# Kernel tuning notes

Measured on AMD Instinct MI355X. Metric: run time of the kernel, lower is better.

Reference implementation:

```python
import jax, jax.numpy as jnp
import numpy as np

K = 3
STRIDE = 1
PADDING = 1


def unfold(x, k, stride, padding):
    # torch.nn.functional.unfold: patches ordered (C, kh, kw), positions row-major
    N, C, H, W = x.shape
    xp = jnp.pad(x, ((0, 0), (0, 0), (padding, padding), (padding, padding)))
    H_out = (H - k + 2 * padding) // stride + 1
    W_out = (W - k + 2 * padding) // stride + 1
    patches = jnp.stack(
        [xp[:, :, i:i + stride * H_out:stride, j:j + stride * W_out:stride]
         for i in range(k) for j in range(k)],
        axis=2,
    )  # (N, C, k*k, H_out, W_out)
    return patches.reshape(N, C * k * k, H_out * W_out), H_out, W_out


def setup_inputs() -> dict:
    key = jax.random.key(0)
    k1, k2 = jax.random.split(key)
    x = jax.random.normal(k1, (16, 64, 14, 14), dtype=jnp.float32)
    W = jax.random.normal(k2, (64, 64, 3, 3), dtype=jnp.float32)
    return {"x": x, "W": W}


def reference(x, W):
    F_out = W.shape[0]
    X_col, H_out, W_out = unfold(x, K, STRIDE, PADDING)  # (N, D, P)
    W_col = W.reshape(F_out, -1)                          # (F, D)
    # AdderNet: out[n,f,p] = -sum_d |W[f,d] - X[n,d,p]|
    out = -jnp.sum(jnp.abs(W_col[None, :, :, None] - X_col[:, None, :, :]), axis=2)  # (N, F, P)
    return out.reshape(x.shape[0], F_out, H_out, W_out)
```

## Files before the change

kernel.cpp:

```cpp
#include <hip/hip_runtime.h>


#define N_ 16
#define C_ 64
#define F_ 64
#define P_ 196
#define CPAD 68
#define NT 4

__global__ __launch_bounds__(256) void adder2d_kernel(
    const float* __restrict__ x, const float* __restrict__ w,
    float* __restrict__ out)
{
    __shared__ __align__(16) float xt[256 * CPAD];

    const int tid = threadIdx.x;
    const int fg  = blockIdx.x;
    const int n   = blockIdx.y;

    float4* xt4 = (float4*)xt;
    #pragma unroll
    for (int i = 0; i < 17; ++i)
        xt4[i * 256 + tid] = make_float4(0.f, 0.f, 0.f, 0.f);
    __syncthreads();

    {
        const int c  = tid & 63;
        const int wq = tid >> 6;
        const float4* x4 = (const float4*)(x + (n * C_ + c) * P_);
        #pragma unroll
        for (int i = 0; i < 13; ++i) {
            const int q = wq + 4 * i;
            if (q < 49) {
                float4 v = x4[q];
                float vv[4] = {v.x, v.y, v.z, v.w};
                const int e = 4 * q;
                #pragma unroll
                for (int j = 0; j < 4; ++j) {
                    const int ee  = e + j;
                    const int r   = ee / 14;
                    const int col = ee - r * 14;
                    xt[((r + 1) * 16 + (col + 1)) * CPAD + c] = vv[j];
                }
            }
        }
    }
    __syncthreads();

    if (tid < P_) {
        const int h  = tid / 14;
        const int wv = tid - h * 14;
        const int fbase = fg * NT;
        const float* wp = w + fbase * (C_ * 9);

        float acc0 = 0.f, acc1 = 0.f, acc2 = 0.f, acc3 = 0.f;
        const float* base = xt + (h * 16 + wv) * CPAD;

        #pragma unroll 2
        for (int g = 0; g < 16; ++g) {
            float4 xv[9];
            #pragma unroll
            for (int kh = 0; kh < 3; ++kh)
                #pragma unroll
                for (int kw = 0; kw < 3; ++kw)
                    xv[kh * 3 + kw] =
                        *(const float4*)(base + (kh * 16 + kw) * CPAD + 4 * g);

            #pragma unroll
            for (int f = 0; f < 4; ++f) {
                const float* wf = wp + f * (C_ * 9) + (4 * g) * 9;
                float a = 0.f;
                #pragma unroll
                for (int kk = 0; kk < 9; ++kk) {
                    a += fabsf(wf[0 * 9 + kk] - xv[kk].x)
                       + fabsf(wf[1 * 9 + kk] - xv[kk].y)
                       + fabsf(wf[2 * 9 + kk] - xv[kk].z)
                       + fabsf(wf[3 * 9 + kk] - xv[kk].w);
                }
                if (f == 0) acc0 += a;
                else if (f == 1) acc1 += a;
                else if (f == 2) acc2 += a;
                else acc3 += a;
            }
        }

        float* op = out + (n * F_ + fbase) * P_ + tid;
        op[0 * P_] = -acc0;
        op[1 * P_] = -acc1;
        op[2 * P_] = -acc2;
        op[3 * P_] = -acc3;
    }
}

extern "C" void kernel_launch(void* const* d_in, const int* in_sizes, int n_in,
                              void* d_out, int out_size, void* d_ws, size_t ws_size,
                              hipStream_t stream) {
    const float* x = (const float*)d_in[0];
    const float* w = (const float*)d_in[1];
    float* out = (float*)d_out;
    dim3 grid(F_ / NT, N_);
    adder2d_kernel<<<grid, 256, 0, stream>>>(x, w, out);
}
```

Measured before the change: 85.32 us.

## Split channel reduction across four thread groups with shared-memory combine

```diff
diff --git a/kernel.cpp b/kernel.cpp
--- a/kernel.cpp
+++ b/kernel.cpp
@@ -8,11 +8,12 @@
 #define CPAD 68
 #define NT 4
 
-__global__ __launch_bounds__(256) void adder2d_kernel(
+__global__ __launch_bounds__(1024) void adder2d_kernel(
     const float* __restrict__ x, const float* __restrict__ w,
     float* __restrict__ out)
 {
     __shared__ __align__(16) float xt[256 * CPAD];
+    __shared__ __align__(16) float4 red[4][256];
 
     const int tid = threadIdx.x;
     const int fg  = blockIdx.x;
@@ -20,17 +21,19 @@
 
     float4* xt4 = (float4*)xt;
     #pragma unroll
-    for (int i = 0; i < 17; ++i)
-        xt4[i * 256 + tid] = make_float4(0.f, 0.f, 0.f, 0.f);
+    for (int i = 0; i < 5; ++i) {
+        int idx = tid + i * 1024;
+        if (idx < 4352) xt4[idx] = make_float4(0.f, 0.f, 0.f, 0.f);
+    }
     __syncthreads();
 
     {
-        const int c  = tid & 63;
-        const int wq = tid >> 6;
+        const int c     = tid & 63;
+        const int phase = tid >> 6;
         const float4* x4 = (const float4*)(x + (n * C_ + c) * P_);
         #pragma unroll
-        for (int i = 0; i < 13; ++i) {
-            const int q = wq + 4 * i;
+        for (int i = 0; i < 4; ++i) {
+            const int q = phase + 16 * i;
             if (q < 49) {
                 float4 v = x4[q];
                 float vv[4] = {v.x, v.y, v.z, v.w};
@@ -47,35 +50,38 @@
     }
     __syncthreads();
 
-    if (tid < P_) {
-        const int h  = tid / 14;
-        const int wv = tid - h * 14;
-        const int fbase = fg * NT;
-        const float* wp = w + fbase * (C_ * 9);
+    const int cq = __builtin_amdgcn_readfirstlane(tid >> 8);
+    const int px = tid & 255;
+    const int fbase = fg * NT;
+    const int cbase = cq * 16;
 
-        float acc0 = 0.f, acc1 = 0.f, acc2 = 0.f, acc3 = 0.f;
-        const float* base = xt + (h * 16 + wv) * CPAD;
+    float acc0 = 0.f, acc1 = 0.f, acc2 = 0.f, acc3 = 0.f;
 
-        #pragma unroll 2
-        for (int g = 0; g < 16; ++g) {
+    if (px < P_) {
+        const int h  = px / 14;
+        const int wv = px - h * 14;
+        const float* bp = xt + (h * 16 + wv) * CPAD + cbase;
+
+        #pragma unroll
+        for (int g = 0; g < 4; ++g) {
+            const float* bg = bp + 4 * g;
             float4 xv[9];
             #pragma unroll
             for (int kh = 0; kh < 3; ++kh)
                 #pragma unroll
                 for (int kw = 0; kw < 3; ++kw)
-                    xv[kh * 3 + kw] =
-                        *(const float4*)(base + (kh * 16 + kw) * CPAD + 4 * g);
+                    xv[kh * 3 + kw] = *(const float4*)(bg + (kh * 16 + kw) * CPAD);
 
             #pragma unroll
             for (int f = 0; f < 4; ++f) {
-                const float* wf = wp + f * (C_ * 9) + (4 * g) * 9;
+                const float* wfp = w + (fbase + f) * (C_ * 9) + (cbase + 4 * g) * 9;
                 float a = 0.f;
                 #pragma unroll
                 for (int kk = 0; kk < 9; ++kk) {
-                    a += fabsf(wf[0 * 9 + kk] - xv[kk].x)
-                       + fabsf(wf[1 * 9 + kk] - xv[kk].y)
-                       + fabsf(wf[2 * 9 + kk] - xv[kk].z)
-                       + fabsf(wf[3 * 9 + kk] - xv[kk].w);
+                    a += fabsf(wfp[0 * 9 + kk] - xv[kk].x)
+                       + fabsf(wfp[1 * 9 + kk] - xv[kk].y)
+                       + fabsf(wfp[2 * 9 + kk] - xv[kk].z)
+                       + fabsf(wfp[3 * 9 + kk] - xv[kk].w);
                 }
                 if (f == 0) acc0 += a;
                 else if (f == 1) acc1 += a;
@@ -83,12 +89,25 @@
                 else acc3 += a;
             }
         }
+    }
 
+    red[cq][px] = make_float4(acc0, acc1, acc2, acc3);
+    __syncthreads();
+
+    if (tid < P_) {
+        float4 r0 = red[0][tid];
+        float4 r1 = red[1][tid];
+        float4 r2 = red[2][tid];
+        float4 r3 = red[3][tid];
+        float o0 = r0.x + r1.x + r2.x + r3.x;
+        float o1 = r0.y + r1.y + r2.y + r3.y;
+        float o2 = r0.z + r1.z + r2.z + r3.z;
+        float o3 = r0.w + r1.w + r2.w + r3.w;
         float* op = out + (n * F_ + fbase) * P_ + tid;
-        op[0 * P_] = -acc0;
-        op[1 * P_] = -acc1;
-        op[2 * P_] = -acc2;
-        op[3 * P_] = -acc3;
+        op[0 * P_] = -o0;
+        op[1 * P_] = -o1;
+        op[2 * P_] = -o2;
+        op[3 * P_] = -o3;
     }
 }
 
@@ -99,5 +118,5 @@
     const float* w = (const float*)d_in[1];
     float* out = (float*)d_out;
     dim3 grid(F_ / NT, N_);
-    adder2d_kernel<<<grid, 256, 0, stream>>>(x, w, out);
+    adder2d_kernel<<<grid, 1024, 0, stream>>>(x, w, out);
 }
```

Result: faster. 69.50 us (-18.5%).

## Split channels across waves and rows across blocks with shared-memory reduction

Applied to the files above, without the earlier changes.

```diff
diff --git a/kernel.cpp b/kernel.cpp
--- a/kernel.cpp
+++ b/kernel.cpp
@@ -6,69 +6,69 @@
 #define F_ 64
 #define P_ 196
 #define CPAD 68
-#define NT 4
+#define ROWS 10
+#define POS (ROWS * 16)
 
-__global__ __launch_bounds__(256) void adder2d_kernel(
+__global__ __launch_bounds__(1024, 8) void adder2d_kernel(
     const float* __restrict__ x, const float* __restrict__ w,
     float* __restrict__ out)
 {
-    __shared__ __align__(16) float xt[256 * CPAD];
+    __shared__ __align__(16) float xt[POS * CPAD];
 
     const int tid = threadIdx.x;
     const int fg  = blockIdx.x;
     const int n   = blockIdx.y;
+    const int hh  = blockIdx.z;
 
     float4* xt4 = (float4*)xt;
     #pragma unroll
-    for (int i = 0; i < 17; ++i)
-        xt4[i * 256 + tid] = make_float4(0.f, 0.f, 0.f, 0.f);
+    for (int i = 0; i < 3; ++i) {
+        int idx = tid + i * 1024;
+        if (idx < POS * CPAD / 4) xt4[idx] = make_float4(0.f, 0.f, 0.f, 0.f);
+    }
     __syncthreads();
 
     {
         const int c  = tid & 63;
-        const int wq = tid >> 6;
-        const float4* x4 = (const float4*)(x + (n * C_ + c) * P_);
+        const int ph = tid >> 6;
+        const float* xc = x + (n * C_ + c) * P_;
         #pragma unroll
-        for (int i = 0; i < 13; ++i) {
-            const int q = wq + 4 * i;
-            if (q < 49) {
-                float4 v = x4[q];
-                float vv[4] = {v.x, v.y, v.z, v.w};
-                const int e = 4 * q;
-                #pragma unroll
-                for (int j = 0; j < 4; ++j) {
-                    const int ee  = e + j;
-                    const int r   = ee / 14;
-                    const int col = ee - r * 14;
-                    xt[((r + 1) * 16 + (col + 1)) * CPAD + c] = vv[j];
-                }
+        for (int i = 0; i < 9; ++i) {
+            const int e = ph + 16 * i;
+            if (e < 140) {
+                const int rl  = e / 14;
+                const int col = e - rl * 14;
+                const int ir  = 6 * hh + rl - 1;
+                if (ir >= 0 && ir <= 13)
+                    xt[(rl * 16 + col + 1) * CPAD + c] = xc[ir * 14 + col];
             }
         }
     }
     __syncthreads();
 
-    if (tid < P_) {
-        const int h  = tid / 14;
-        const int wv = tid - h * 14;
-        const int fbase = fg * NT;
-        const float* wp = w + fbase * (C_ * 9);
+    const int cq  = __builtin_amdgcn_readfirstlane(tid >> 7);
+    const int pxl = tid & 127;
+    float a0 = 0.f, a1 = 0.f, a2 = 0.f, a3 = 0.f;
 
-        float acc0 = 0.f, acc1 = 0.f, acc2 = 0.f, acc3 = 0.f;
-        const float* base = xt + (h * 16 + wv) * CPAD;
+    if (pxl < 98) {
+        const int rr  = pxl / 14;
+        const int col = pxl - rr * 14;
+        const float* base = xt + ((hh + rr) * 16 + col) * CPAD + cq * 8;
+        const int fbase = fg * 4;
 
-        #pragma unroll 2
-        for (int g = 0; g < 16; ++g) {
+        #pragma unroll 1
+        for (int g = 0; g < 2; ++g) {
             float4 xv[9];
             #pragma unroll
             for (int kh = 0; kh < 3; ++kh)
                 #pragma unroll
                 for (int kw = 0; kw < 3; ++kw)
                     xv[kh * 3 + kw] =
-                        *(const float4*)(base + (kh * 16 + kw) * CPAD + 4 * g);
+                        *(const float4*)(base + g * 4 + (kh * 16 + kw) * CPAD);
 
             #pragma unroll
             for (int f = 0; f < 4; ++f) {
-                const float* wf = wp + f * (C_ * 9) + (4 * g) * 9;
+                const float* wf = w + (fbase + f) * (C_ * 9) + (cq * 8 + g * 4) * 9;
                 float a = 0.f;
                 #pragma unroll
                 for (int kk = 0; kk < 9; ++kk) {
@@ -77,18 +77,33 @@
                        + fabsf(wf[2 * 9 + kk] - xv[kk].z)
                        + fabsf(wf[3 * 9 + kk] - xv[kk].w);
                 }
-                if (f == 0) acc0 += a;
-                else if (f == 1) acc1 += a;
-                else if (f == 2) acc2 += a;
-                else acc3 += a;
+                if (f == 0) a0 += a;
+                else if (f == 1) a1 += a;
+                else if (f == 2) a2 += a;
+                else a3 += a;
             }
         }
+    }
 
-        float* op = out + (n * F_ + fbase) * P_ + tid;
-        op[0 * P_] = -acc0;
-        op[1 * P_] = -acc1;
-        op[2 * P_] = -acc2;
-        op[3 * P_] = -acc3;
+    __syncthreads();
+    ((float4*)xt)[cq * 128 + pxl] = make_float4(a0, a1, a2, a3);
+    __syncthreads();
+
+    if (tid < 98) {
+        float4 t = make_float4(0.f, 0.f, 0.f, 0.f);
+        #pragma unroll
+        for (int j = 0; j < 8; ++j) {
+            float4 r = ((float4*)xt)[j * 128 + tid];
+            t.x += r.x; t.y += r.y; t.z += r.z; t.w += r.w;
+        }
+        const int rr  = tid / 14;
+        const int col = tid - rr * 14;
+        const int ro  = 7 * hh + rr;
+        float* op = out + (n * F_ + fg * 4) * P_ + ro * 14 + col;
+        op[0 * P_] = -t.x;
+        op[1 * P_] = -t.y;
+        op[2 * P_] = -t.z;
+        op[3 * P_] = -t.w;
     }
 }
 
@@ -98,6 +113,6 @@
     const float* x = (const float*)d_in[0];
     const float* w = (const float*)d_in[1];
     float* out = (float*)d_out;
-    dim3 grid(F_ / NT, N_);
-    adder2d_kernel<<<grid, 256, 0, stream>>>(x, w, out);
+    dim3 grid(F_ / 4, N_, 2);
+    adder2d_kernel<<<grid, 1024, 0, stream>>>(x, w, out);
 }
```

Result: slower. 97.51 us (+14.3%).
